# Optimization experiments

Hardware: AMD Instinct MI355X
Metric: run time of the kernel (lower is better)

Reference implementation:

```python
import jax, jax.numpy as jnp
import numpy as np


def _leaky(x, s):
    return jnp.where(x >= 0, x, s * x)


def _conv2d(x, w, b=None):
    y = jax.lax.conv_general_dilated(x, w, (1, 1), 'VALID',
                                     dimension_numbers=('NCHW', 'OIHW', 'NCHW'))
    if b is not None:
        y = y + b[None, :, None, None]
    return y


def _bn(x, g, b, m, v):
    # eval-mode BatchNorm2d with running stats, eps=1e-5
    inv = jax.lax.rsqrt(v + 1e-5)
    return (x - m[None, :, None, None]) * (g * inv)[None, :, None, None] + b[None, :, None, None]


def setup_inputs() -> dict:
    key = jax.random.key(0)
    ks = jax.random.split(key, 16)
    B, C, H, W = 1024, 103, 15, 15
    F, N = 64, 4
    r = lambda k, shp: jax.random.normal(k, shp, dtype=jnp.float32) * 0.05
    return {
        'x': jax.random.normal(ks[0], (B, C, H, W), dtype=jnp.float32),
        'conv1_w': r(ks[1], (32, C, 3, 3)), 'conv1_b': r(ks[2], (32,)),
        'bn1_g': jnp.ones((32,), jnp.float32), 'bn1_b': jnp.zeros((32,), jnp.float32),
        'bn1_m': jnp.zeros((32,), jnp.float32), 'bn1_v': jnp.ones((32,), jnp.float32),
        'conv2_w': r(ks[3], (64, 32, 3, 3)), 'conv2_b': r(ks[4], (64,)),
        'bn2_g': jnp.ones((64,), jnp.float32), 'bn2_b': jnp.zeros((64,), jnp.float32),
        'bn2_m': jnp.zeros((64,), jnp.float32), 'bn2_v': jnp.ones((64,), jnp.float32),
        'fc_sam_w': r(ks[5], (N, 64)),
        'conv_t_w': r(ks[6], (F, 64)), 'conv_t_b': r(ks[7], (F,)),
        's_adj_w': r(ks[8], (N, N)),
        's_w_w': r(ks[9], (F, F)), 's_w_b': r(ks[10], (F,)),
        'd_co_w': r(ks[11], (N, 2 * F)), 'd_co_b': r(ks[12], (N,)),
        'd_gamma': jnp.zeros((1,), jnp.float32),
        'd_dw_w': r(ks[13], (F, F)), 'd_dw_b': r(ks[14], (F,)),
    }


def reference(x, conv1_w, conv1_b, bn1_g, bn1_b, bn1_m, bn1_v,
              conv2_w, conv2_b, bn2_g, bn2_b, bn2_m, bn2_v,
              fc_sam_w, conv_t_w, conv_t_b, s_adj_w, s_w_w, s_w_b,
              d_co_w, d_co_b, d_gamma, d_dw_w, d_dw_b):
    B = x.shape[0]
    # backbone (eval mode: DropBlock is identity)
    x1 = _bn(_leaky(_conv2d(x, conv1_w, conv1_b), 0.01), bn1_g, bn1_b, bn1_m, bn1_v)
    x2 = _bn(_leaky(_conv2d(x1, conv2_w, conv2_b), 0.01), bn2_g, bn2_b, bn2_m, bn2_v)
    # SAM: [B,64,H*W] features, [B,num_node,H*W] sigmoid mask, matmul -> [B,64,num_node]
    flat = x2.reshape(B, x2.shape[1], -1)  # [B,64,L]
    mask = jax.nn.sigmoid(jnp.einsum('nc,bcl->bnl', fc_sam_w, flat))  # [B,N,L]
    xt = jnp.einsum('oc,bcl->bol', conv_t_w, flat) + conv_t_b[None, :, None]
    x3 = jnp.einsum('bcl,bnl->bcn', xt, mask)  # [B,F,N]
    # SGraph: static adjacency (conv1d over node dim) + static weight (conv1d over feature dim)
    a = _leaky(jnp.einsum('mn,bfn->bfm', s_adj_w, x3), 0.2)  # [B,F,N]
    sg = _leaky(jnp.einsum('of,bfn->bon', s_w_w, a) + s_w_b[None, :, None], 0.2)
    x4 = sg + x3
    # DGraph: self-attention over channels -> dynamic adjacency over nodes
    energy = jnp.einsum('bcn,bdn->bcd', x4, x4)  # [B,F,F]
    e_new = jnp.max(energy, axis=-1, keepdims=True) - energy
    att = jax.nn.softmax(e_new, axis=-1)
    out = jnp.einsum('bcd,bdn->bcn', att, x4)
    x_glb = d_gamma[0] * out + x4
    cat = jnp.concatenate([x_glb, x4], axis=1)  # [B,2F,N]
    dadj = jax.nn.sigmoid(jnp.einsum('mk,bkn->bmn', d_co_w, cat) + d_co_b[None, :, None])  # [B,N,N]
    y = _leaky(jnp.einsum('bcn,bnm->bcm', x4, dadj), 0.2)
    y = _leaky(jnp.einsum('of,bfn->bon', d_dw_w, y) + d_dw_b[None, :, None], 0.2)
    x5 = y + x4
    x6 = x5.reshape(B, -1)  # [B, F*N]
    return (x6, x2)
```

## Files before the change

kernel.cpp:

```cpp
#include <hip/hip_runtime.h>
#include <math.h>

typedef __bf16 bf16x8 __attribute__((ext_vector_type(8)));
typedef float f32x4 __attribute__((ext_vector_type(4)));

#define LEAKY1(v) ((v) >= 0.f ? (v) : 0.01f*(v))
#define LEAKY2(v) ((v) >= 0.f ? (v) : 0.2f*(v))

__device__ __forceinline__ unsigned short f2bf(float f) {
  unsigned u = __float_as_uint(f);
  u += 0x7FFFu + ((u >> 16) & 1u);
  return (unsigned short)(u >> 16);
}

__global__ void w1prep_kernel(const float* __restrict__ w, unsigned short* __restrict__ w1p) {
  int idx = blockIdx.x * 256 + threadIdx.x;
  if (idx >= 9 * 32 * 128) return;
  int tap = idx >> 12;
  int rem = idx & 4095;
  int oc  = rem >> 7;
  int k   = rem & 127;
  int ky = tap / 3, kx = tap - ky * 3;
  unsigned short v = 0;
  if (k < 103) v = f2bf(w[((oc * 103 + k) * 3 + ky) * 3 + kx]);
  w1p[idx] = v;
}

__global__ void w2prep_kernel(const float* __restrict__ w, unsigned short* __restrict__ w2p) {
  int idx = blockIdx.x * 256 + threadIdx.x;
  if (idx >= 9 * 64 * 32) return;
  int tap = idx >> 11;
  int rem = idx & 2047;
  int oc  = rem >> 5;
  int k   = rem & 31;
  int ky = tap / 3, kx = tap - ky * 3;
  w2p[idx] = f2bf(w[((oc * 32 + k) * 3 + ky) * 3 + kx]);
}

__global__ void w3prep_kernel(const float* __restrict__ ctw, const float* __restrict__ fcw,
                              unsigned short* __restrict__ w3p) {
  int idx = blockIdx.x * 256 + threadIdx.x;
  if (idx >= 80 * 64) return;
  int row = idx >> 6, c = idx & 63;
  float v = 0.f;
  if (row < 64) v = ctw[row * 64 + c];
  else if (row < 68) v = fcw[(row - 64) * 64 + c];
  w3p[idx] = f2bf(v);
}

__global__ __launch_bounds__(256) void conv1_mfma(
    const float* __restrict__ x, const unsigned short* __restrict__ w1p,
    const float* __restrict__ cb, const float* __restrict__ bng,
    const float* __restrict__ bnb, const float* __restrict__ bnm,
    const float* __restrict__ bnv, unsigned short* __restrict__ x1g) {
  __shared__ __align__(16) unsigned short im[23448];
  const int b_  = blockIdx.x;
  const int tid = threadIdx.x;
  const float* xin = x + (size_t)b_ * 23175;

  for (int i = tid; i < 225; i += 256) im[i * 104 + 103] = 0;
  for (int i = tid; i < 48; i += 256) im[23400 + i] = 0;

  if (tid < 225) {
    const float* src = xin + tid;
    unsigned short* dst = im + tid * 104;
#pragma unroll 8
    for (int ic = 0; ic < 103; ++ic) dst[ic] = f2bf(src[(size_t)ic * 225]);
  }
  __syncthreads();

  const int lane = tid & 63, wid = tid >> 6;
  const int ln = lane & 15, kg = lane >> 4;

  int rb[3], pv[3];
#pragma unroll
  for (int nt = 0; nt < 3; ++nt) {
    int pix = (wid * 3 + nt) * 16 + ln;
    pv[nt] = (pix < 169);
    if (pix >= 169) pix = 0;
    int oy = pix / 13, ox = pix - oy * 13;
    rb[nt] = (oy * 15 + ox) * 208 + kg * 16;
  }

  f32x4 acc[2][3];
#pragma unroll
  for (int mt = 0; mt < 2; ++mt)
#pragma unroll
    for (int nt = 0; nt < 3; ++nt) acc[mt][nt] = (f32x4){0.f, 0.f, 0.f, 0.f};

  const unsigned short* wbase = w1p + (size_t)ln * 128 + kg * 8;
  const char* imb = (const char*)im;

  for (int ky = 0; ky < 3; ++ky) {
    for (int kx = 0; kx < 3; ++kx) {
      const int tap = ky * 3 + kx;
      const int tsh = (ky * 15 + kx) * 208;
      const unsigned short* wp = wbase + tap * 4096;
      bf16x8 a0[4], a1[4];
#pragma unroll
      for (int kt = 0; kt < 4; ++kt) {
        a0[kt] = *(const bf16x8*)(wp + kt * 32);
        a1[kt] = *(const bf16x8*)(wp + 2048 + kt * 32);
      }
#pragma unroll
      for (int kt = 0; kt < 4; ++kt) {
#pragma unroll
        for (int nt = 0; nt < 3; ++nt) {
          bf16x8 bv = *(const bf16x8*)(imb + rb[nt] + tsh + kt * 64);
          acc[0][nt] = __builtin_amdgcn_mfma_f32_16x16x32_bf16(a0[kt], bv, acc[0][nt], 0, 0, 0);
          acc[1][nt] = __builtin_amdgcn_mfma_f32_16x16x32_bf16(a1[kt], bv, acc[1][nt], 0, 0, 0);
        }
      }
    }
  }

#pragma unroll
  for (int mt = 0; mt < 2; ++mt) {
#pragma unroll
    for (int nt = 0; nt < 3; ++nt) {
      if (!pv[nt]) continue;
      int pix = (wid * 3 + nt) * 16 + ln;
      unsigned short* dst = x1g + ((size_t)b_ * 169 + pix) * 32;
      f32x4 a = acc[mt][nt];
#pragma unroll
      for (int r = 0; r < 4; ++r) {
        int oc = mt * 16 + kg * 4 + r;
        float val = a[r] + cb[oc];
        val = LEAKY1(val);
        float sc = bng[oc] * rsqrtf(bnv[oc] + 1e-5f);
        float sh = bnb[oc] - bnm[oc] * sc;
        dst[oc] = f2bf(val * sc + sh);
      }
    }
  }
}

__global__ __launch_bounds__(256) void conv2_mfma(
    const unsigned short* __restrict__ x1g, const unsigned short* __restrict__ w2p,
    const float* __restrict__ cb, const float* __restrict__ bng,
    const float* __restrict__ bnb, const float* __restrict__ bnm,
    const float* __restrict__ bnv, float* __restrict__ x2out) {
  __shared__ __align__(16) unsigned short im2[6760];
  const int b_  = blockIdx.x;
  const int tid = threadIdx.x;

  for (int i = tid; i < 676; i += 256) {
    int pix = i >> 2, icg = i & 3;
    const uint4* src = (const uint4*)(x1g + ((size_t)b_ * 169 + pix) * 32 + icg * 8);
    *(uint4*)(im2 + pix * 40 + icg * 8) = *src;
  }
  __syncthreads();

  const int lane = tid & 63, wid = tid >> 6;
  const int ln = lane & 15, kg = lane >> 4;

  int rb[2], pv[2];
#pragma unroll
  for (int nt = 0; nt < 2; ++nt) {
    int pix = (wid * 2 + nt) * 16 + ln;
    pv[nt] = (pix < 121);
    if (pix >= 121) pix = 0;
    int oy = pix / 11, ox = pix - oy * 11;
    rb[nt] = (oy * 13 + ox) * 80 + kg * 16;
  }

  f32x4 acc[4][2];
#pragma unroll
  for (int mt = 0; mt < 4; ++mt)
#pragma unroll
    for (int nt = 0; nt < 2; ++nt) acc[mt][nt] = (f32x4){0.f, 0.f, 0.f, 0.f};

  const unsigned short* wbase = w2p + (size_t)ln * 32 + kg * 8;
  const char* imb = (const char*)im2;

  for (int ky = 0; ky < 3; ++ky) {
    for (int kx = 0; kx < 3; ++kx) {
      const int tap = ky * 3 + kx;
      const int tsh = (ky * 13 + kx) * 80;
      const unsigned short* wp = wbase + tap * 2048;
      bf16x8 a[4];
#pragma unroll
      for (int mt = 0; mt < 4; ++mt) a[mt] = *(const bf16x8*)(wp + mt * 512);
#pragma unroll
      for (int nt = 0; nt < 2; ++nt) {
        bf16x8 bv = *(const bf16x8*)(imb + rb[nt] + tsh);
#pragma unroll
        for (int mt = 0; mt < 4; ++mt)
          acc[mt][nt] = __builtin_amdgcn_mfma_f32_16x16x32_bf16(a[mt], bv, acc[mt][nt], 0, 0, 0);
      }
    }
  }

#pragma unroll
  for (int mt = 0; mt < 4; ++mt) {
#pragma unroll
    for (int nt = 0; nt < 2; ++nt) {
      if (!pv[nt]) continue;
      int pix = (wid * 2 + nt) * 16 + ln;
      f32x4 a = acc[mt][nt];
#pragma unroll
      for (int r = 0; r < 4; ++r) {
        int oc = mt * 16 + kg * 4 + r;
        float val = a[r] + cb[oc];
        val = LEAKY1(val);
        float sc = bng[oc] * rsqrtf(bnv[oc] + 1e-5f);
        float sh = bnb[oc] - bnm[oc] * sc;
        x2out[((size_t)b_ * 64 + oc) * 121 + pix] = val * sc + sh;
      }
    }
  }
}

__global__ __launch_bounds__(256) void sam_graph_kernel(
    const float* __restrict__ x2,
    const unsigned short* __restrict__ w3p,
    const float* __restrict__ conv_t_b,
    const float* __restrict__ s_adj_w,
    const float* __restrict__ s_w_w,
    const float* __restrict__ s_w_b,
    const float* __restrict__ d_co_w,
    const float* __restrict__ d_co_b,
    const float* __restrict__ d_gamma,
    const float* __restrict__ d_dw_w,
    const float* __restrict__ d_dw_b,
    float* __restrict__ x6) {
  __shared__ __align__(16) unsigned short s_flatT[128][72];
  __shared__ __align__(16) unsigned short s_xt[64][136];
  __shared__ __align__(16) unsigned short s_mask[16][136];
  __shared__ float s_x3[64][4];
  __shared__ float s_a[64][4];
  __shared__ float s_x4[64][4];
  __shared__ float s_att[64][66];
  __shared__ float s_xg[64][4];
  __shared__ float s_dadj[4][4];
  __shared__ float s_y[64][4];

  const int b   = blockIdx.x;
  const int tid = threadIdx.x;
  const float* f = x2 + (size_t)b * 7744;

  for (int i = tid; i < 7 * 72; i += 256) s_flatT[121 + i / 72][i % 72] = 0;
  for (int i = tid; i < 16 * 136; i += 256) (&s_mask[0][0])[i] = 0;

  for (int i = tid; i < 7744; i += 256) {
    int c = i / 121, l = i - c * 121;
    s_flatT[l][c] = f2bf(f[i]);
  }
  __syncthreads();

  const int lane = tid & 63, wid = tid >> 6;
  const int ln = lane & 15, kg = lane >> 4;

  for (int t = wid * 10; t < wid * 10 + 10; ++t) {
    const int mt = t >> 3, nt = t & 7;
    f32x4 acc = (f32x4){0.f, 0.f, 0.f, 0.f};
#pragma unroll
    for (int k0 = 0; k0 < 64; k0 += 32) {
      bf16x8 af = *(const bf16x8*)(w3p + (mt * 16 + ln) * 64 + k0 + kg * 8);
      bf16x8 bf_ = *(const bf16x8*)(&s_flatT[nt * 16 + ln][k0 + kg * 8]);
      acc = __builtin_amdgcn_mfma_f32_16x16x32_bf16(af, bf_, acc, 0, 0, 0);
    }
    const int l = nt * 16 + ln;
#pragma unroll
    for (int r = 0; r < 4; ++r) {
      int row = mt * 16 + kg * 4 + r;
      if (row < 64) s_xt[row][l] = f2bf(acc[r] + conv_t_b[row]);
      else if (row < 68) s_mask[row - 64][l] = f2bf(1.f / (1.f + __expf(-acc[r])));
    }
  }
  __syncthreads();
  if (tid < 28) s_mask[tid / 7][121 + tid % 7] = 0;
  __syncthreads();

  {
    f32x4 acc = (f32x4){0.f, 0.f, 0.f, 0.f};
#pragma unroll
    for (int k0 = 0; k0 < 128; k0 += 32) {
      bf16x8 af = *(const bf16x8*)(&s_xt[wid * 16 + ln][k0 + kg * 8]);
      bf16x8 bf_ = *(const bf16x8*)(&s_mask[ln][k0 + kg * 8]);
      acc = __builtin_amdgcn_mfma_f32_16x16x32_bf16(af, bf_, acc, 0, 0, 0);
    }
    if (ln < 4) {
#pragma unroll
      for (int r = 0; r < 4; ++r) s_x3[wid * 16 + kg * 4 + r][ln] = acc[r];
    }
  }
  __syncthreads();

  {
    int fi = tid >> 2, m = tid & 3;
    float s = 0.f;
#pragma unroll
    for (int n = 0; n < 4; ++n) s = fmaf(s_adj_w[m * 4 + n], s_x3[fi][n], s);
    s_a[fi][m] = LEAKY2(s);
  }
  __syncthreads();

  {
    int o = tid >> 2, n = tid & 3;
    float s = s_w_b[o];
    for (int ff = 0; ff < 64; ++ff) s = fmaf(s_w_w[o * 64 + ff], s_a[ff][n], s);
    s = LEAKY2(s);
    s_x4[o][n] = s + s_x3[o][n];
  }
  __syncthreads();

  for (int i = tid; i < 4096; i += 256) {
    int c = i >> 6, d = i & 63;
    float s = 0.f;
#pragma unroll
    for (int n = 0; n < 4; ++n) s = fmaf(s_x4[c][n], s_x4[d][n], s);
    s_att[c][d] = s;
  }
  __syncthreads();

  if (tid < 64) {
    int c = tid;
    float mn = 1e30f;
    for (int d = 0; d < 64; ++d) mn = fminf(mn, s_att[c][d]);
    float ssum = 0.f;
    for (int d = 0; d < 64; ++d) {
      float e = __expf(mn - s_att[c][d]);
      s_att[c][d] = e;
      ssum += e;
    }
    float inv = 1.f / ssum;
    for (int d = 0; d < 64; ++d) s_att[c][d] *= inv;
  }
  __syncthreads();

  const float gamma = d_gamma[0];
  {
    int c = tid >> 2, n = tid & 3;
    float s = 0.f;
    for (int d = 0; d < 64; ++d) s = fmaf(s_att[c][d], s_x4[d][n], s);
    s_xg[c][n] = gamma * s + s_x4[c][n];
  }
  __syncthreads();

  if (tid < 16) {
    int m = tid >> 2, n = tid & 3;
    float s = d_co_b[m];
    for (int k = 0; k < 64; ++k) s = fmaf(d_co_w[m * 128 + k],      s_xg[k][n], s);
    for (int k = 0; k < 64; ++k) s = fmaf(d_co_w[m * 128 + 64 + k], s_x4[k][n], s);
    s_dadj[m][n] = 1.f / (1.f + __expf(-s));
  }
  __syncthreads();

  {
    int c = tid >> 2, m = tid & 3;
    float s = 0.f;
#pragma unroll
    for (int n = 0; n < 4; ++n) s = fmaf(s_x4[c][n], s_dadj[n][m], s);
    s_y[c][m] = LEAKY2(s);
  }
  __syncthreads();

  {
    int o = tid >> 2, n = tid & 3;
    float s = d_dw_b[o];
    for (int ff = 0; ff < 64; ++ff) s = fmaf(d_dw_w[o * 64 + ff], s_y[ff][n], s);
    s = LEAKY2(s);
    x6[(size_t)b * 256 + tid] = s + s_x4[o][n];
  }
}

extern "C" void kernel_launch(void* const* d_in, const int* in_sizes, int n_in,
                              void* d_out, int out_size, void* d_ws, size_t ws_size,
                              hipStream_t stream) {
  const float* x     = (const float*)d_in[0];
  const float* c1w   = (const float*)d_in[1];
  const float* c1b   = (const float*)d_in[2];
  const float* bn1g  = (const float*)d_in[3];
  const float* bn1b  = (const float*)d_in[4];
  const float* bn1m  = (const float*)d_in[5];
  const float* bn1v  = (const float*)d_in[6];
  const float* c2w   = (const float*)d_in[7];
  const float* c2b   = (const float*)d_in[8];
  const float* bn2g  = (const float*)d_in[9];
  const float* bn2b  = (const float*)d_in[10];
  const float* bn2m  = (const float*)d_in[11];
  const float* bn2v  = (const float*)d_in[12];
  const float* fcw   = (const float*)d_in[13];
  const float* ctw   = (const float*)d_in[14];
  const float* ctb   = (const float*)d_in[15];
  const float* sadj  = (const float*)d_in[16];
  const float* sww   = (const float*)d_in[17];
  const float* swb   = (const float*)d_in[18];
  const float* dcow  = (const float*)d_in[19];
  const float* dcob  = (const float*)d_in[20];
  const float* dgam  = (const float*)d_in[21];
  const float* ddww  = (const float*)d_in[22];
  const float* ddwb  = (const float*)d_in[23];

  float* out = (float*)d_out;
  float* x6  = out;
  float* x2  = out + (size_t)1024 * 256;

  unsigned short* x1g = (unsigned short*)d_ws;
  unsigned short* w1p = x1g + (size_t)1024 * 169 * 32;
  unsigned short* w2p = w1p + 9 * 32 * 128;
  unsigned short* w3p = w2p + 9 * 64 * 32;

  w1prep_kernel<<<144, 256, 0, stream>>>(c1w, w1p);
  w2prep_kernel<<<72, 256, 0, stream>>>(c2w, w2p);
  w3prep_kernel<<<20, 256, 0, stream>>>(ctw, fcw, w3p);
  conv1_mfma<<<1024, 256, 0, stream>>>(x, w1p, c1b, bn1g, bn1b, bn1m, bn1v, x1g);
  conv2_mfma<<<1024, 256, 0, stream>>>(x1g, w2p, c2b, bn2g, bn2b, bn2m, bn2v, x2);
  sam_graph_kernel<<<1024, 256, 0, stream>>>(x2, w3p, ctb, sadj, sww, swb,
                                             dcow, dcob, dgam, ddww, ddwb, x6);
}
```

Baseline: 307.3 us.

## Fuse conv2 with SAM/graph kernel and batch conv1 input loads

Merges the conv2 kernel and the SAM/graph kernel into one, writing conv2 results as bf16 straight into shared memory (transposed flat layout) while still storing x2 to global, so the second kernel no longer re-reads x2 from global and converts it. Shared memory is overlaid between phases to fit. The conv1 input staging loop is also restructured to issue 16 loads at once and store packed ushort4s. The fused kernel uses more shared memory and registers per block, which may reduce occupancy.

```diff
diff --git a/kernel.cpp b/kernel.cpp
--- a/kernel.cpp
+++ b/kernel.cpp
@@ -64,8 +64,26 @@
   if (tid < 225) {
     const float* src = xin + tid;
     unsigned short* dst = im + tid * 104;
-#pragma unroll 8
-    for (int ic = 0; ic < 103; ++ic) dst[ic] = f2bf(src[(size_t)ic * 225]);
+    int ic = 0;
+    for (; ic + 16 <= 103; ic += 16) {
+      float v[16];
+#pragma unroll
+      for (int u = 0; u < 16; ++u) v[u] = src[(size_t)(ic + u) * 225];
+#pragma unroll
+      for (int u = 0; u < 16; u += 4) {
+        ushort4 q;
+        q.x = f2bf(v[u]); q.y = f2bf(v[u + 1]);
+        q.z = f2bf(v[u + 2]); q.w = f2bf(v[u + 3]);
+        *(ushort4*)(dst + ic + u) = q;
+      }
+    }
+    {
+      float v[7];
+#pragma unroll
+      for (int u = 0; u < 7; ++u) v[u] = src[(size_t)(96 + u) * 225];
+#pragma unroll
+      for (int u = 0; u < 7; ++u) dst[96 + u] = f2bf(v[u]);
+    }
   }
   __syncthreads();
 
@@ -135,15 +153,37 @@
   }
 }
 
-__global__ __launch_bounds__(256) void conv2_mfma(
+__global__ __launch_bounds__(256) void conv2_sam(
     const unsigned short* __restrict__ x1g, const unsigned short* __restrict__ w2p,
     const float* __restrict__ cb, const float* __restrict__ bng,
     const float* __restrict__ bnb, const float* __restrict__ bnm,
-    const float* __restrict__ bnv, float* __restrict__ x2out) {
-  __shared__ __align__(16) unsigned short im2[6760];
+    const float* __restrict__ bnv,
+    const unsigned short* __restrict__ w3p,
+    const float* __restrict__ conv_t_b,
+    const float* __restrict__ s_adj_w, const float* __restrict__ s_w_w,
+    const float* __restrict__ s_w_b,
+    const float* __restrict__ d_co_w, const float* __restrict__ d_co_b,
+    const float* __restrict__ d_gamma,
+    const float* __restrict__ d_dw_w, const float* __restrict__ d_dw_b,
+    float* __restrict__ x2out, float* __restrict__ x6) {
+  __shared__ __align__(16) char smem[45440];
+  unsigned short* im2    = (unsigned short*)smem;
+  unsigned short* s_xt   = (unsigned short*)smem;
+  unsigned short* s_flatT = (unsigned short*)(smem + 17408);
+  float*          s_att   = (float*)(smem + 17408);
+  unsigned short* s_mask = (unsigned short*)(smem + 35840);
+  float* s_x3   = (float*)(smem + 40192);
+  float* s_a    = s_x3 + 256;
+  float* s_x4   = s_a + 256;
+  float* s_xg   = s_x4 + 256;
+  float* s_y    = s_xg + 256;
+  float* s_dadj = s_y + 256;
+
   const int b_  = blockIdx.x;
   const int tid = threadIdx.x;
 
+  for (int i = tid; i < 252; i += 256) ((int*)(s_flatT + 121 * 72))[i] = 0;
+  for (int i = tid; i < 1088; i += 256) ((int*)s_mask)[i] = 0;
   for (int i = tid; i < 676; i += 256) {
     int pix = i >> 2, icg = i & 3;
     const uint4* src = (const uint4*)(x1g + ((size_t)b_ * 169 + pix) * 32 + icg * 8);
@@ -164,29 +204,30 @@
     rb[nt] = (oy * 13 + ox) * 80 + kg * 16;
   }
 
-  f32x4 acc[4][2];
+  f32x4 acc2[4][2];
 #pragma unroll
   for (int mt = 0; mt < 4; ++mt)
 #pragma unroll
-    for (int nt = 0; nt < 2; ++nt) acc[mt][nt] = (f32x4){0.f, 0.f, 0.f, 0.f};
-
-  const unsigned short* wbase = w2p + (size_t)ln * 32 + kg * 8;
-  const char* imb = (const char*)im2;
-
-  for (int ky = 0; ky < 3; ++ky) {
-    for (int kx = 0; kx < 3; ++kx) {
-      const int tap = ky * 3 + kx;
-      const int tsh = (ky * 13 + kx) * 80;
-      const unsigned short* wp = wbase + tap * 2048;
-      bf16x8 a[4];
-#pragma unroll
-      for (int mt = 0; mt < 4; ++mt) a[mt] = *(const bf16x8*)(wp + mt * 512);
-#pragma unroll
-      for (int nt = 0; nt < 2; ++nt) {
-        bf16x8 bv = *(const bf16x8*)(imb + rb[nt] + tsh);
-#pragma unroll
-        for (int mt = 0; mt < 4; ++mt)
-          acc[mt][nt] = __builtin_amdgcn_mfma_f32_16x16x32_bf16(a[mt], bv, acc[mt][nt], 0, 0, 0);
+    for (int nt = 0; nt < 2; ++nt) acc2[mt][nt] = (f32x4){0.f, 0.f, 0.f, 0.f};
+
+  {
+    const unsigned short* wbase = w2p + (size_t)ln * 32 + kg * 8;
+    const char* imb = (const char*)im2;
+    for (int ky = 0; ky < 3; ++ky) {
+      for (int kx = 0; kx < 3; ++kx) {
+        const int tap = ky * 3 + kx;
+        const int tsh = (ky * 13 + kx) * 80;
+        const unsigned short* wp = wbase + tap * 2048;
+        bf16x8 a[4];
+#pragma unroll
+        for (int mt = 0; mt < 4; ++mt) a[mt] = *(const bf16x8*)(wp + mt * 512);
+#pragma unroll
+        for (int nt = 0; nt < 2; ++nt) {
+          bf16x8 bv = *(const bf16x8*)(imb + rb[nt] + tsh);
+#pragma unroll
+          for (int mt = 0; mt < 4; ++mt)
+            acc2[mt][nt] = __builtin_amdgcn_mfma_f32_16x16x32_bf16(a[mt], bv, acc2[mt][nt], 0, 0, 0);
+        }
       }
     }
   }
@@ -197,7 +238,9 @@
     for (int nt = 0; nt < 2; ++nt) {
       if (!pv[nt]) continue;
       int pix = (wid * 2 + nt) * 16 + ln;
-      f32x4 a = acc[mt][nt];
+      f32x4 a = acc2[mt][nt];
+      ushort4 q;
+      float vv[4];
 #pragma unroll
       for (int r = 0; r < 4; ++r) {
         int oc = mt * 16 + kg * 4 + r;
@@ -205,51 +248,14 @@
         val = LEAKY1(val);
         float sc = bng[oc] * rsqrtf(bnv[oc] + 1e-5f);
         float sh = bnb[oc] - bnm[oc] * sc;
-        x2out[((size_t)b_ * 64 + oc) * 121 + pix] = val * sc + sh;
-      }
-    }
-  }
-}
-
-__global__ __launch_bounds__(256) void sam_graph_kernel(
-    const float* __restrict__ x2,
-    const unsigned short* __restrict__ w3p,
-    const float* __restrict__ conv_t_b,
-    const float* __restrict__ s_adj_w,
-    const float* __restrict__ s_w_w,
-    const float* __restrict__ s_w_b,
-    const float* __restrict__ d_co_w,
-    const float* __restrict__ d_co_b,
-    const float* __restrict__ d_gamma,
-    const float* __restrict__ d_dw_w,
-    const float* __restrict__ d_dw_b,
-    float* __restrict__ x6) {
-  __shared__ __align__(16) unsigned short s_flatT[128][72];
-  __shared__ __align__(16) unsigned short s_xt[64][136];
-  __shared__ __align__(16) unsigned short s_mask[16][136];
-  __shared__ float s_x3[64][4];
-  __shared__ float s_a[64][4];
-  __shared__ float s_x4[64][4];
-  __shared__ float s_att[64][66];
-  __shared__ float s_xg[64][4];
-  __shared__ float s_dadj[4][4];
-  __shared__ float s_y[64][4];
-
-  const int b   = blockIdx.x;
-  const int tid = threadIdx.x;
-  const float* f = x2 + (size_t)b * 7744;
-
-  for (int i = tid; i < 7 * 72; i += 256) s_flatT[121 + i / 72][i % 72] = 0;
-  for (int i = tid; i < 16 * 136; i += 256) (&s_mask[0][0])[i] = 0;
-
-  for (int i = tid; i < 7744; i += 256) {
-    int c = i / 121, l = i - c * 121;
-    s_flatT[l][c] = f2bf(f[i]);
-  }
-  __syncthreads();
-
-  const int lane = tid & 63, wid = tid >> 6;
-  const int ln = lane & 15, kg = lane >> 4;
+        vv[r] = val * sc + sh;
+        x2out[((size_t)b_ * 64 + oc) * 121 + pix] = vv[r];
+      }
+      q.x = f2bf(vv[0]); q.y = f2bf(vv[1]); q.z = f2bf(vv[2]); q.w = f2bf(vv[3]);
+      *(ushort4*)(s_flatT + pix * 72 + mt * 16 + kg * 4) = q;
+    }
+  }
+  __syncthreads();
 
   for (int t = wid * 10; t < wid * 10 + 10; ++t) {
     const int mt = t >> 3, nt = t & 7;
@@ -257,32 +263,32 @@
 #pragma unroll
     for (int k0 = 0; k0 < 64; k0 += 32) {
       bf16x8 af = *(const bf16x8*)(w3p + (mt * 16 + ln) * 64 + k0 + kg * 8);
-      bf16x8 bf_ = *(const bf16x8*)(&s_flatT[nt * 16 + ln][k0 + kg * 8]);
+      bf16x8 bf_ = *(const bf16x8*)(s_flatT + (nt * 16 + ln) * 72 + k0 + kg * 8);
       acc = __builtin_amdgcn_mfma_f32_16x16x32_bf16(af, bf_, acc, 0, 0, 0);
     }
     const int l = nt * 16 + ln;
 #pragma unroll
     for (int r = 0; r < 4; ++r) {
       int row = mt * 16 + kg * 4 + r;
-      if (row < 64) s_xt[row][l] = f2bf(acc[r] + conv_t_b[row]);
-      else if (row < 68) s_mask[row - 64][l] = f2bf(1.f / (1.f + __expf(-acc[r])));
-    }
-  }
-  __syncthreads();
-  if (tid < 28) s_mask[tid / 7][121 + tid % 7] = 0;
+      if (row < 64) s_xt[row * 136 + l] = f2bf(acc[r] + conv_t_b[row]);
+      else if (row < 68) s_mask[(row - 64) * 136 + l] = f2bf(1.f / (1.f + __expf(-acc[r])));
+    }
+  }
+  __syncthreads();
+  if (tid < 28) s_mask[(tid / 7) * 136 + 121 + tid % 7] = 0;
   __syncthreads();
 
   {
     f32x4 acc = (f32x4){0.f, 0.f, 0.f, 0.f};
 #pragma unroll
     for (int k0 = 0; k0 < 128; k0 += 32) {
-      bf16x8 af = *(const bf16x8*)(&s_xt[wid * 16 + ln][k0 + kg * 8]);
-      bf16x8 bf_ = *(const bf16x8*)(&s_mask[ln][k0 + kg * 8]);
+      bf16x8 af = *(const bf16x8*)(s_xt + (wid * 16 + ln) * 136 + k0 + kg * 8);
+      bf16x8 bf_ = *(const bf16x8*)(s_mask + ln * 136 + k0 + kg * 8);
       acc = __builtin_amdgcn_mfma_f32_16x16x32_bf16(af, bf_, acc, 0, 0, 0);
     }
     if (ln < 4) {
 #pragma unroll
-      for (int r = 0; r < 4; ++r) s_x3[wid * 16 + kg * 4 + r][ln] = acc[r];
+      for (int r = 0; r < 4; ++r) s_x3[(wid * 16 + kg * 4 + r) * 4 + ln] = acc[r];
     }
   }
   __syncthreads();
@@ -291,17 +297,17 @@
     int fi = tid >> 2, m = tid & 3;
     float s = 0.f;
 #pragma unroll
-    for (int n = 0; n < 4; ++n) s = fmaf(s_adj_w[m * 4 + n], s_x3[fi][n], s);
-    s_a[fi][m] = LEAKY2(s);
+    for (int n = 0; n < 4; ++n) s = fmaf(s_adj_w[m * 4 + n], s_x3[fi * 4 + n], s);
+    s_a[fi * 4 + m] = LEAKY2(s);
   }
   __syncthreads();
 
   {
     int o = tid >> 2, n = tid & 3;
     float s = s_w_b[o];
-    for (int ff = 0; ff < 64; ++ff) s = fmaf(s_w_w[o * 64 + ff], s_a[ff][n], s);
+    for (int ff = 0; ff < 64; ++ff) s = fmaf(s_w_w[o * 64 + ff], s_a[ff * 4 + n], s);
     s = LEAKY2(s);
-    s_x4[o][n] = s + s_x3[o][n];
+    s_x4[o * 4 + n] = s + s_x3[o * 4 + n];
   }
   __syncthreads();
 
@@ -309,23 +315,23 @@
     int c = i >> 6, d = i & 63;
     float s = 0.f;
 #pragma unroll
-    for (int n = 0; n < 4; ++n) s = fmaf(s_x4[c][n], s_x4[d][n], s);
-    s_att[c][d] = s;
+    for (int n = 0; n < 4; ++n) s = fmaf(s_x4[c * 4 + n], s_x4[d * 4 + n], s);
+    s_att[c * 66 + d] = s;
   }
   __syncthreads();
 
   if (tid < 64) {
-    int c = tid;
+    float* row = s_att + tid * 66;
     float mn = 1e30f;
-    for (int d = 0; d < 64; ++d) mn = fminf(mn, s_att[c][d]);
+    for (int d = 0; d < 64; ++d) mn = fminf(mn, row[d]);
     float ssum = 0.f;
     for (int d = 0; d < 64; ++d) {
-      float e = __expf(mn - s_att[c][d]);
-      s_att[c][d] = e;
+      float e = __expf(mn - row[d]);
+      row[d] = e;
       ssum += e;
     }
     float inv = 1.f / ssum;
-    for (int d = 0; d < 64; ++d) s_att[c][d] *= inv;
+    for (int d = 0; d < 64; ++d) row[d] *= inv;
   }
   __syncthreads();
 
@@ -333,17 +339,17 @@
   {
     int c = tid >> 2, n = tid & 3;
     float s = 0.f;
-    for (int d = 0; d < 64; ++d) s = fmaf(s_att[c][d], s_x4[d][n], s);
-    s_xg[c][n] = gamma * s + s_x4[c][n];
+    for (int d = 0; d < 64; ++d) s = fmaf(s_att[c * 66 + d], s_x4[d * 4 + n], s);
+    s_xg[c * 4 + n] = gamma * s + s_x4[c * 4 + n];
   }
   __syncthreads();
 
   if (tid < 16) {
     int m = tid >> 2, n = tid & 3;
     float s = d_co_b[m];
-    for (int k = 0; k < 64; ++k) s = fmaf(d_co_w[m * 128 + k],      s_xg[k][n], s);
-    for (int k = 0; k < 64; ++k) s = fmaf(d_co_w[m * 128 + 64 + k], s_x4[k][n], s);
-    s_dadj[m][n] = 1.f / (1.f + __expf(-s));
+    for (int k = 0; k < 64; ++k) s = fmaf(d_co_w[m * 128 + k],      s_xg[k * 4 + n], s);
+    for (int k = 0; k < 64; ++k) s = fmaf(d_co_w[m * 128 + 64 + k], s_x4[k * 4 + n], s);
+    s_dadj[m * 4 + n] = 1.f / (1.f + __expf(-s));
   }
   __syncthreads();
 
@@ -351,17 +357,17 @@
     int c = tid >> 2, m = tid & 3;
     float s = 0.f;
 #pragma unroll
-    for (int n = 0; n < 4; ++n) s = fmaf(s_x4[c][n], s_dadj[n][m], s);
-    s_y[c][m] = LEAKY2(s);
+    for (int n = 0; n < 4; ++n) s = fmaf(s_x4[c * 4 + n], s_dadj[n * 4 + m], s);
+    s_y[c * 4 + m] = LEAKY2(s);
   }
   __syncthreads();
 
   {
     int o = tid >> 2, n = tid & 3;
     float s = d_dw_b[o];
-    for (int ff = 0; ff < 64; ++ff) s = fmaf(d_dw_w[o * 64 + ff], s_y[ff][n], s);
+    for (int ff = 0; ff < 64; ++ff) s = fmaf(d_dw_w[o * 64 + ff], s_y[ff * 4 + n], s);
     s = LEAKY2(s);
-    x6[(size_t)b * 256 + tid] = s + s_x4[o][n];
+    x6[(size_t)b_ * 256 + tid] = s + s_x4[tid];
   }
 }
 
@@ -406,7 +412,7 @@
   w2prep_kernel<<<72, 256, 0, stream>>>(c2w, w2p);
   w3prep_kernel<<<20, 256, 0, stream>>>(ctw, fcw, w3p);
   conv1_mfma<<<1024, 256, 0, stream>>>(x, w1p, c1b, bn1g, bn1b, bn1m, bn1v, x1g);
-  conv2_mfma<<<1024, 256, 0, stream>>>(x1g, w2p, c2b, bn2g, bn2b, bn2m, bn2v, x2);
-  sam_graph_kernel<<<1024, 256, 0, stream>>>(x2, w3p, ctb, sadj, sww, swb,
-                                             dcow, dcob, dgam, ddww, ddwb, x6);
-}
+  conv2_sam<<<1024, 256, 0, stream>>>(x1g, w2p, c2b, bn2g, bn2b, bn2m, bn2v,
+                                      w3p, ctb, sadj, sww, swb, dcow, dcob, dgam,
+                                      ddww, ddwb, x2, x6);
+}
```

Measured after the change: 285.9 us. 1.07x faster.
